# Performance work log

Hardware: AMD Instinct MI355X
Metric: run time of the kernel (lower is better)

## Reference

```python
import jax, jax.numpy as jnp
import numpy as np

HIDDEN = 512
HEADS = 8
HEAD_DIM = HIDDEN // HEADS
MAX_DIST = 10
B, N = 16, 512
EPS = 1e-5


def _layer_norm(x, g, b):
    mu = jnp.mean(x, axis=-1, keepdims=True)
    var = jnp.mean(jnp.square(x - mu), axis=-1, keepdims=True)
    return (x - mu) * jax.lax.rsqrt(var + EPS) * g + b


def setup_inputs() -> dict:
    key = jax.random.key(0)
    ks = jax.random.split(key, 16)
    s = 0.02
    inp = {
        "x": jax.random.normal(ks[0], (B, N, HIDDEN), jnp.float32),
        "distances": jax.random.randint(ks[1], (B, N, N), 0, MAX_DIST, jnp.int32),
        "edge_features": jax.random.normal(ks[2], (B, N, N), jnp.float32),
        "attn_mask": jax.random.randint(ks[3], (B, N), 0, 2).astype(bool),
        "Wq": jax.random.normal(ks[4], (HIDDEN, HIDDEN), jnp.float32) * s,
        "bq": jnp.zeros((HIDDEN,), jnp.float32),
        "Wk": jax.random.normal(ks[5], (HIDDEN, HIDDEN), jnp.float32) * s,
        "bk": jnp.zeros((HIDDEN,), jnp.float32),
        "Wv": jax.random.normal(ks[6], (HIDDEN, HIDDEN), jnp.float32) * s,
        "bv": jnp.zeros((HIDDEN,), jnp.float32),
        "Wo": jax.random.normal(ks[7], (HIDDEN, HIDDEN), jnp.float32) * s,
        "bo": jnp.zeros((HIDDEN,), jnp.float32),
        "spatial_emb": jax.random.normal(ks[8], (MAX_DIST, HEADS), jnp.float32) * s,
        "edge_w": jax.random.normal(ks[9], (HEADS,), jnp.float32) * s,
        "edge_b": jnp.zeros((HEADS,), jnp.float32),
        "ln1_g": jnp.ones((HIDDEN,), jnp.float32),
        "ln1_b": jnp.zeros((HIDDEN,), jnp.float32),
        "ln2_g": jnp.ones((HIDDEN,), jnp.float32),
        "ln2_b": jnp.zeros((HIDDEN,), jnp.float32),
        "W1": jax.random.normal(ks[10], (HIDDEN, 4 * HIDDEN), jnp.float32) * s,
        "b1": jnp.zeros((4 * HIDDEN,), jnp.float32),
        "W2": jax.random.normal(ks[11], (4 * HIDDEN, HIDDEN), jnp.float32) * s,
        "b2": jnp.zeros((HIDDEN,), jnp.float32),
    }
    return inp


def reference(x, distances, edge_features, attn_mask, Wq, bq, Wk, bk, Wv, bv,
              Wo, bo, spatial_emb, edge_w, edge_b, ln1_g, ln1_b, ln2_g, ln2_b,
              W1, b1, W2, b2):
    b, n, _ = x.shape
    q = (x @ Wq + bq).reshape(b, n, HEADS, HEAD_DIM)
    k = (x @ Wk + bk).reshape(b, n, HEADS, HEAD_DIM)
    v = (x @ Wv + bv).reshape(b, n, HEADS, HEAD_DIM)
    # [b, h, i, j] attention scores
    scores = jnp.einsum('bihd,bjhd->bhij', q, k) / np.sqrt(HEAD_DIM).astype(np.float32)
    spatial_bias = spatial_emb[distances]                       # [b, i, j, h]
    edge_bias = edge_features[..., None] * edge_w + edge_b      # [b, i, j, h]
    scores = scores + jnp.transpose(spatial_bias + edge_bias, (0, 3, 1, 2))
    scores = jnp.where(attn_mask[:, None, None, :], -jnp.inf, scores)
    attn = jax.nn.softmax(scores, axis=-1)
    out = jnp.einsum('bhij,bjhd->bihd', attn, v).reshape(b, n, HIDDEN)
    out = out @ Wo + bo
    h = _layer_norm(x + out, ln1_g, ln1_b)
    ffn = jax.nn.relu(h @ W1 + b1) @ W2 + b2
    return _layer_norm(h + ffn, ln2_g, ln2_b)
```

## Files before the change

### kernel.cpp

```cpp
#include <hip/hip_runtime.h>
#include <stdint.h>
#include <stddef.h>

#define SEQ   512
#define HID   512
#define NHEAD 8
#define HD    64
#define NBATCH 16
#define NTOK  8192
#define MAXD  10
#define LOG2E 1.4426950408889634f

typedef __attribute__((ext_vector_type(8))) short short8;
typedef __attribute__((ext_vector_type(4))) float f32x4;

typedef __attribute__((address_space(3))) void        as3_void;
typedef const __attribute__((address_space(1))) void  as1_cvoid;

#define MFMA16(a,b,c) __builtin_amdgcn_mfma_f32_16x16x32_bf16((a),(b),(c),0,0,0)

__device__ __forceinline__ float bf2f(uint16_t u){ return __uint_as_float(((uint32_t)u)<<16); }
__device__ __forceinline__ uint16_t f2bf(float f){
  uint32_t i = __float_as_uint(f);
  return (uint16_t)((i + 0x7fffu + ((i>>16)&1u)) >> 16);
}

enum { EPI_BF16=0, EPI_F32=3, EPI_RELU=4 };

__global__ __launch_bounds__(256) void f2bf_kernel(
    const float* __restrict__ in, uint16_t* __restrict__ out, int n4)
{
  int i = blockIdx.x*256 + threadIdx.x;
  if (i < n4){
    float4 v = *(const float4*)(in + (size_t)i*4);
    *(ushort4*)(out + (size_t)i*4) =
        make_ushort4(f2bf(v.x), f2bf(v.y), f2bf(v.z), f2bf(v.w));
  }
}

__global__ __launch_bounds__(256) void transpose_all(
    const float* __restrict__ Wq, const float* __restrict__ Wk,
    const float* __restrict__ Wv, const float* __restrict__ Wo,
    const float* __restrict__ W1, const float* __restrict__ W2,
    uint16_t* __restrict__ tq, uint16_t* __restrict__ tk,
    uint16_t* __restrict__ tv, uint16_t* __restrict__ to_,
    uint16_t* __restrict__ t1, uint16_t* __restrict__ t2)
{
  __shared__ uint16_t tile[32][33];
  int id = blockIdx.x;
  const float* in; uint16_t* out; int R, C, tx, ty;
  if (id < 1024) {
    int m = id >> 8, loc = id & 255;
    in  = (m==0)?Wq:(m==1)?Wk:(m==2)?Wv:Wo;
    out = (m==0)?tq:(m==1)?tk:(m==2)?tv:to_;
    R = 512; C = 512; ty = loc>>4; tx = loc&15;
  } else if (id < 2048) {
    int loc = id-1024; in=W1; out=t1; R=512; C=2048; ty=loc>>6; tx=loc&63;
  } else {
    int loc = id-2048; in=W2; out=t2; R=2048; C=512; ty=loc>>4; tx=loc&15;
  }
  int bx = tx*32, by = ty*32;
  int lx = threadIdx.x & 31, ly = threadIdx.x >> 5;
  #pragma unroll
  for (int i=ly; i<32; i+=8) tile[i][lx] = f2bf(in[(size_t)(by+i)*C + bx+lx]);
  __syncthreads();
  #pragma unroll
  for (int i=ly; i<32; i+=8) out[(size_t)(bx+i)*R + by+lx] = tile[lx][i];
}

__global__ __launch_bounds__(512) void pack_bias(
    const int*   __restrict__ dist,
    const float* __restrict__ edge,
    const int*   __restrict__ mask,
    uint32_t*    __restrict__ outp)
{
  __shared__ int   dl[16][260];
  __shared__ float el[16][260];
  __shared__ int   ml[512];
  const int b  = blockIdx.y;
  const int it = blockIdx.x;
  const int t  = threadIdx.x;
  ml[t] = mask[b*SEQ + t];

  #pragma unroll
  for (int jh=0; jh<2; ++jh){
    if (jh) __syncthreads();
    {
      const int r  = t >> 5;
      const int c0 = (t & 31) * 8;
      const size_t g = ((size_t)b*SEQ + it*16 + r)*SEQ + jh*256 + c0;
      *(int4*)&dl[r][c0]     = *(const int4*)&dist[g];
      *(int4*)&dl[r][c0+4]   = *(const int4*)&dist[g+4];
      *(float4*)&el[r][c0]   = *(const float4*)&edge[g];
      *(float4*)&el[r][c0+4] = *(const float4*)&edge[g+4];
    }
    __syncthreads();
    {
      const int i   = t & 15;
      const int j0p = (t >> 4) * 8;
      const int jt  = jh*4 + (j0p >> 6);
      const int jn  = (j0p >> 4) & 3;
      const int lg  = (j0p & 15) >> 2;
      uint32_t w[8];
      #pragma unroll
      for (int e=0; e<8; ++e){
        const int jl = j0p + e;
        const int jg = jh*256 + jl;
        const uint32_t d  = (uint32_t)dl[i][jl] & 0xFFu;
        const uint32_t mk = (ml[jg] ? 1u : 0u) << 8;
        w[e] = ((uint32_t)f2bf(el[i][jl]) << 16) | mk | d;
      }
      uint32_t* ob = outp + ((((size_t)b*32 + it)*8 + jt)*64)*16;
      const int lane0 = lg*16 + i, lane1 = (lg+1)*16 + i;
      *(uint4*)&ob[lane0*16 + jn*4] = make_uint4(w[0],w[1],w[2],w[3]);
      *(uint4*)&ob[lane1*16 + jn*4] = make_uint4(w[4],w[5],w[6],w[7]);
    }
  }
}

template<int BM, int BN>
__device__ __forceinline__ void gemm_tile_mainloop(
    const uint16_t* __restrict__ A, const uint16_t* __restrict__ Bt,
    int K, int m0, int n0, uint16_t* lA, uint16_t* lB,
    f32x4 acc[4][(BM==128)?4:((BN==128)?2:1)])
{
  constexpr int NJ  = (BM==128)?4:((BN==128)?2:1);
  constexpr int ARD = BM/32;
  constexpr int BRD = BN/32;
  constexpr bool DB = (BM==64) && (BN==64);
  const int t = threadIdx.x;
  const int w = t>>6, l = t&63;
  const int lg = l>>4, lc = l&15;
  const int wr = (BM==128)?(w>>1):0;
  const int wc = (BM==128)?(w&1):w;
  const int swz = lc & 7;
  const int kSteps = K>>6;

  auto stage = [&](int kt, int buf){
    const int k0 = kt<<6;
    #pragma unroll
    for (int rd=0; rd<ARD; ++rd){
      const int e   = rd*2048 + t*8;
      const int row = e>>6;
      const int col = (((e>>3)&7) ^ (row&7))*8;
      const uint16_t* ga = A + (size_t)(m0+row)*K + (k0+col);
      char* la = (char*)(lA + buf*(BM*64)) + rd*4096 + w*1024;
      __builtin_amdgcn_global_load_lds((as1_cvoid*)ga, (as3_void*)la, 16, 0, 0);
    }
    #pragma unroll
    for (int rd=0; rd<BRD; ++rd){
      const int e   = rd*2048 + t*8;
      const int row = e>>6;
      const int col = (((e>>3)&7) ^ (row&7))*8;
      const uint16_t* gb = Bt + (size_t)(n0+row)*K + (k0+col);
      char* lb = (char*)(lB + buf*(BN*64)) + rd*4096 + w*1024;
      __builtin_amdgcn_global_load_lds((as1_cvoid*)gb, (as3_void*)lb, 16, 0, 0);
    }
  };

  auto compute = [&](const uint16_t* rA, const uint16_t* rB){
    #pragma unroll
    for (int kk=0; kk<2; ++kk){
      const int cc = (kk*4 + lg) ^ swz;
      short8 af[4], bfr[NJ];
      #pragma unroll
      for (int i=0;i<4;i++)
        af[i]  = *(const short8*)&rA[(wr*64 + i*16 + lc)*64 + cc*8];
      #pragma unroll
      for (int j=0;j<NJ;j++)
        bfr[j] = *(const short8*)&rB[(wc*16*NJ + j*16 + lc)*64 + cc*8];
      #pragma unroll
      for (int i=0;i<4;i++)
        #pragma unroll
        for (int j=0;j<NJ;j++)
          acc[i][j] = MFMA16(af[i], bfr[j], acc[i][j]);
    }
  };

  if constexpr (DB){
    stage(0, 0);
    __syncthreads();
    int cur = 0;
    for (int kt=0; kt<kSteps; ++kt){
      if (kt+1 < kSteps) stage(kt+1, cur^1);
      compute(lA + cur*(BM*64), lB + cur*(BN*64));
      __syncthreads();
      cur ^= 1;
    }
  } else {
    for (int kt=0; kt<kSteps; ++kt){
      stage(kt, 0);
      __syncthreads();
      compute(lA, lB);
      __syncthreads();
    }
  }
}

template<int EPI, int BM, int BN>
__global__ __launch_bounds__(256,2) void gemm_bt(
    const uint16_t* __restrict__ A, const uint16_t* __restrict__ Bt,
    const float* __restrict__ bias, void* __restrict__ outp,
    int M, int N, int K)
{
  constexpr int NJ = (BM==128)?4:((BN==128)?2:1);
  constexpr int NB = ((BM==64)&&(BN==64)) ? 2 : 1;
  __shared__ uint16_t lA[NB*BM*64];
  __shared__ uint16_t lB[NB*BN*64];
  f32x4 acc[4][NJ];
  #pragma unroll
  for (int i=0;i<4;i++)
    #pragma unroll
    for (int j=0;j<NJ;j++){ f32x4 z = {0.f,0.f,0.f,0.f}; acc[i][j]=z; }
  const int m0 = blockIdx.x*BM, n0 = blockIdx.y*BN;
  gemm_tile_mainloop<BM,BN>(A, Bt, K, m0, n0, lA, lB, acc);

  const int t=threadIdx.x, w=t>>6, l=t&63, lg=l>>4, lc=l&15;
  const int wr=(BM==128)?(w>>1):0, wc=(BM==128)?(w&1):w;
  #pragma unroll
  for (int j=0;j<NJ;j++){
    const int col = n0 + wc*16*NJ + j*16 + lc;
    const float bs = bias[col];
    #pragma unroll
    for (int i=0;i<4;i++){
      const int rowb = m0 + wr*64 + i*16 + lg*4;
      #pragma unroll
      for (int r=0;r<4;r++){
        float v = acc[i][j][r] + bs;
        if constexpr (EPI==EPI_RELU)   v = fmaxf(v, 0.f);
        if constexpr (EPI==EPI_F32)
          ((float*)outp)[(size_t)(rowb+r)*N + col] = v;
        else
          ((uint16_t*)outp)[(size_t)(rowb+r)*N + col] = f2bf(v);
      }
    }
  }
}

__global__ __launch_bounds__(256,2) void qkv_gemm(
    const uint16_t* __restrict__ x,
    const uint16_t* __restrict__ wtq, const uint16_t* __restrict__ wtk,
    const uint16_t* __restrict__ wtv,
    const float* __restrict__ bq, const float* __restrict__ bk,
    const float* __restrict__ bv,
    uint16_t* __restrict__ qo, uint16_t* __restrict__ kp,
    uint16_t* __restrict__ vp)
{
  __shared__ uint16_t lA[2*64*64];
  __shared__ uint16_t lB[2*64*64];
  const int z = blockIdx.z;
  const uint16_t* Bt = (z==0)?wtq:(z==1)?wtk:wtv;
  const float*  bias = (z==0)?bq :(z==1)?bk :bv;
  f32x4 acc[4][1];
  #pragma unroll
  for (int i=0;i<4;i++){ f32x4 zz = {0.f,0.f,0.f,0.f}; acc[i][0]=zz; }
  const int m0 = blockIdx.x*64, n0 = blockIdx.y*64;
  gemm_tile_mainloop<64,64>(x, Bt, HID, m0, n0, lA, lB, acc);

  const int t=threadIdx.x, w=t>>6, l=t&63, lg=l>>4, lc=l&15;
  const int col = n0 + w*16 + lc;
  if (z==0){
    const float scale = 0.125f * LOG2E;
    const float bs = bias[col];
    #pragma unroll
    for (int i=0;i<4;i++){
      const int rowb = m0 + i*16 + lg*4;
      #pragma unroll
      for (int r=0;r<4;r++)
        qo[(size_t)(rowb+r)*HID + col] = f2bf((acc[i][0][r] + bs)*scale);
    }
  } else if (z==1){
    const float bs = bias[col];
    const int h_ = col>>6, cm = col&63, kk = cm>>5, lgk = (cm>>3)&3, e = col&7;
    #pragma unroll
    for (int i=0;i<4;i++){
      const int rowb = m0 + i*16 + lg*4;
      #pragma unroll
      for (int r=0;r<4;r++){
        const int tok = rowb + r;
        const int b_ = tok>>9, tl = tok&511;
        const int jt = tl>>6, jn = (tl>>4)&3, lck = tl&15;
        kp[((((size_t)(b_*8+h_)*8 + jt)*4 + jn)*2 + kk)*512
           + (lgk*16 + lck)*8 + e] = f2bf(acc[i][0][r] + bs);
      }
    }
  } else {
    const float bs = bias[col];
    const int h_ = col>>6, dn = (col>>4)&3, lcv = col&15;
    #pragma unroll
    for (int i=0;i<4;i++){
      const int rowb = m0 + i*16 + lg*4;
      const int b_ = rowb>>9, tl = rowb&511;
      const int jt = tl>>6, kk = (tl>>5)&1, lgv = (tl>>3)&3, e0 = tl&7;
      *(ushort4*)&vp[((((size_t)(b_*8+h_)*8 + jt)*2 + kk)*4 + dn)*512
                     + (lgv*16 + lcv)*8 + e0] =
          make_ushort4(f2bf(acc[i][0][0]+bs), f2bf(acc[i][0][1]+bs),
                       f2bf(acc[i][0][2]+bs), f2bf(acc[i][0][3]+bs));
    }
  }
}

__global__ __launch_bounds__(512,4) void attn_kernel(
    const uint16_t* __restrict__ q,
    const uint16_t* __restrict__ kp,
    const uint16_t* __restrict__ vp,
    const uint32_t* __restrict__ biasp,
    const float*    __restrict__ semb,
    const float*    __restrict__ ew,
    const float*    __restrict__ eb,
    uint16_t* __restrict__ out)
{
  __shared__ float sp_rep[NHEAD][32][11];
  __shared__ uint16_t plds[NHEAD][2][16*72];
  const int b  = blockIdx.y;
  const int it = blockIdx.x;
  const int i0 = it*16;
  const int t  = threadIdx.x;
  const int h  = t>>6, l = t&63, lg = l>>4, lc = l&15;
  for (int i = t; i < NHEAD*32*MAXD; i += 512){
    const int hh = i / (32*MAXD), rem = i % (32*MAXD);
    const int a = rem / MAXD, d = rem % MAXD;
    sp_rep[hh][a][d] = (semb[d*NHEAD + hh] + eb[hh]) * LOG2E;
  }
  __syncthreads();
  const float ewf = ew[h] * LOG2E;
  const float* spl = &sp_rep[h][l&31][0];
  char* pbase = (char*)&plds[h][0][0] + lc*144;

  short8 qf[2];
  #pragma unroll
  for (int kk=0;kk<2;kk++)
    qf[kk] = *(const short8*)&q[(size_t)(b*SEQ + i0 + lc)*HID + h*HD + kk*32 + lg*8];

  const uint4* bp = (const uint4*)(biasp + (((size_t)b*32 + it)*8)*64*16);
  const uint16_t* kpb = kp + (size_t)(b*8+h)*8*4*2*512 + l*8;
  const uint16_t* vpb = vp + (size_t)(b*8+h)*8*2*4*512 + l*8;

  float mrun[2] = {-1e30f, -1e30f};
  float lrun[2] = {0.f, 0.f};
  f32x4 oacc[2][4];
  #pragma unroll
  for (int s=0;s<2;s++)
    #pragma unroll
    for (int dn=0;dn<4;dn++){ f32x4 z={0.f,0.f,0.f,0.f}; oacc[s][dn]=z; }

  #pragma unroll
  for (int p=0; p<4; ++p){
    #pragma unroll
    for (int s=0; s<2; ++s){
      const int jt = s*4 + p;
      uint32_t uw[16];
      {
        const uint4* bq_ = bp + (jt*64 + l)*4;
        *(uint4*)&uw[0]  = bq_[0];
        *(uint4*)&uw[4]  = bq_[1];
        *(uint4*)&uw[8]  = bq_[2];
        *(uint4*)&uw[12] = bq_[3];
      }
      f32x4 st[4];
      #pragma unroll
      for (int jn=0;jn<4;jn++){ f32x4 z={0.f,0.f,0.f,0.f}; st[jn]=z; }
      __builtin_amdgcn_s_setprio(1);
      #pragma unroll
      for (int jn=0;jn<4;jn++){
        #pragma unroll
        for (int kk=0;kk<2;kk++){
          short8 kf = *(const short8*)&kpb[(size_t)((jt*4 + jn)*2 + kk)*512];
          st[jn] = MFMA16(kf, qf[kk], st[jn]);
        }
      }
      __builtin_amdgcn_s_setprio(0);
      float tmax = -1e30f;
      #pragma unroll
      for (int jn=0;jn<4;jn++){
        #pragma unroll
        for (int r=0;r<4;r++){
          const uint32_t u = uw[jn*4+r];
          float sv = st[jn][r] + spl[u & 0xFFu]
                   + bf2f((uint16_t)(u >> 16))*ewf;
          if (u & 0x100u) sv = -1e30f;
          st[jn][r] = sv;
          tmax = fmaxf(tmax, sv);
        }
      }
      {
        float tm = fmaxf(tmax, __shfl_xor(tmax, 16, 64));
        tm = fmaxf(tm, __shfl_xor(tm, 32, 64));
        float mnew = fmaxf(mrun[s], tm);
        mnew = fmaxf(mnew, -1e20f);
        const float c = __builtin_amdgcn_exp2f(mrun[s] - mnew);
        mrun[s] = mnew;
        float lsum = 0.f;
        char* pb = pbase + s*(16*72*2);
        #pragma unroll
        for (int jn=0;jn<4;jn++){
          float p0 = __builtin_amdgcn_exp2f(st[jn][0]-mnew);
          float p1 = __builtin_amdgcn_exp2f(st[jn][1]-mnew);
          float p2 = __builtin_amdgcn_exp2f(st[jn][2]-mnew);
          float p3 = __builtin_amdgcn_exp2f(st[jn][3]-mnew);
          lsum += (p0+p1)+(p2+p3);
          *(ushort4*)(pb + (jn*16 + lg*4)*2) =
              make_ushort4(f2bf(p0), f2bf(p1), f2bf(p2), f2bf(p3));
        }
        lrun[s] = lrun[s]*c + lsum;
        #pragma unroll
        for (int r=0;r<4;r++){
          const float cr = __shfl(c, lg*4+r, 64);
          #pragma unroll
          for (int dn=0;dn<4;dn++) oacc[s][dn][r] *= cr;
        }
      }
    }
    #pragma unroll
    for (int s=0; s<2; ++s){
      const int jt = s*4 + p;
      char* pb = pbase + s*(16*72*2);
      __builtin_amdgcn_s_setprio(1);
      #pragma unroll
      for (int kk=0;kk<2;kk++){
        short8 pa = *(const short8*)(pb + (kk*32 + lg*8)*2);
        #pragma unroll
        for (int dn=0;dn<4;dn++){
          short8 vb = *(const short8*)&vpb[(size_t)((jt*2 + kk)*4 + dn)*512];
          oacc[s][dn] = MFMA16(pa, vb, oacc[s][dn]);
        }
      }
      __builtin_amdgcn_s_setprio(0);
    }
  }
  {
    const float mm = fmaxf(mrun[0], mrun[1]);
    const float c0 = __builtin_amdgcn_exp2f(mrun[0]-mm);
    const float c1 = __builtin_amdgcn_exp2f(mrun[1]-mm);
    float ls = lrun[0]*c0 + lrun[1]*c1;
    ls += __shfl_xor(ls, 16, 64);
    ls += __shfl_xor(ls, 32, 64);
    const float inv = 1.f/ls;
    #pragma unroll
    for (int r=0;r<4;r++){
      const float cr0 = __shfl(c0, lg*4+r, 64);
      const float cr1 = __shfl(c1, lg*4+r, 64);
      const float ir  = __shfl(inv, lg*4+r, 64);
      const size_t orow = ((size_t)b*SEQ + i0 + lg*4 + r)*HID;
      #pragma unroll
      for (int dn=0;dn<4;dn++)
        out[orow + h*HD + dn*16 + lc] =
            f2bf((oacc[0][dn][r]*cr0 + oacc[1][dn][r]*cr1)*ir);
    }
  }
}

__global__ __launch_bounds__(256) void ln_kernel(
    const uint16_t* __restrict__ a, const float* __restrict__ bsrc,
    const float* __restrict__ g, const float* __restrict__ bb,
    float* __restrict__ of, uint16_t* __restrict__ ob)
{
  const int row = blockIdx.x*4 + (threadIdx.x>>6);
  const int l = threadIdx.x & 63;
  const int c0 = l*8;
  const uint16_t* ar = a    + (size_t)row*HID + c0;
  const float*    br = bsrc + (size_t)row*HID + c0;
  short8 av = *(const short8*)ar;
  float4 b0 = *(const float4*)br;
  float4 b1 = *(const float4*)(br+4);
  float u[8];
  u[0]=bf2f((uint16_t)av[0])+b0.x; u[1]=bf2f((uint16_t)av[1])+b0.y;
  u[2]=bf2f((uint16_t)av[2])+b0.z; u[3]=bf2f((uint16_t)av[3])+b0.w;
  u[4]=bf2f((uint16_t)av[4])+b1.x; u[5]=bf2f((uint16_t)av[5])+b1.y;
  u[6]=bf2f((uint16_t)av[6])+b1.z; u[7]=bf2f((uint16_t)av[7])+b1.w;
  float s=0.f, ss=0.f;
  #pragma unroll
  for (int e=0;e<8;e++){ s += u[e]; ss += u[e]*u[e]; }
  #pragma unroll
  for (int off=32; off>=1; off>>=1){
    s  += __shfl_xor(s,  off, 64);
    ss += __shfl_xor(ss, off, 64);
  }
  const float mu  = s*(1.f/512.f);
  const float inv = rsqrtf(ss*(1.f/512.f) - mu*mu + 1e-5f);
  float4 g0 = *(const float4*)(g + c0),  g1 = *(const float4*)(g + c0 + 4);
  float4 q0 = *(const float4*)(bb + c0), q1 = *(const float4*)(bb + c0 + 4);
  float y[8];
  y[0]=(u[0]-mu)*inv*g0.x+q0.x; y[1]=(u[1]-mu)*inv*g0.y+q0.y;
  y[2]=(u[2]-mu)*inv*g0.z+q0.z; y[3]=(u[3]-mu)*inv*g0.w+q0.w;
  y[4]=(u[4]-mu)*inv*g1.x+q1.x; y[5]=(u[5]-mu)*inv*g1.y+q1.y;
  y[6]=(u[6]-mu)*inv*g1.z+q1.z; y[7]=(u[7]-mu)*inv*g1.w+q1.w;
  if (of){
    float* orow = of + (size_t)row*HID + c0;
    *(float4*)orow     = make_float4(y[0],y[1],y[2],y[3]);
    *(float4*)(orow+4) = make_float4(y[4],y[5],y[6],y[7]);
  }
  if (ob){
    uint16_t* brow = ob + (size_t)row*HID + c0;
    *(ushort4*)brow     = make_ushort4(f2bf(y[0]),f2bf(y[1]),f2bf(y[2]),f2bf(y[3]));
    *(ushort4*)(brow+4) = make_ushort4(f2bf(y[4]),f2bf(y[5]),f2bf(y[6]),f2bf(y[7]));
  }
}

extern "C" void kernel_launch(void* const* d_in, const int* in_sizes, int n_in,
                              void* d_out, int out_size, void* d_ws, size_t ws_size,
                              hipStream_t stream)
{
  (void)in_sizes; (void)n_in; (void)out_size; (void)ws_size;
  const float* x    = (const float*)d_in[0];
  const int*   dist = (const int*)  d_in[1];
  const float* edge = (const float*)d_in[2];
  const int*   mask = (const int*)  d_in[3];
  const float* Wq = (const float*)d_in[4];
  const float* bq = (const float*)d_in[5];
  const float* Wk = (const float*)d_in[6];
  const float* bk = (const float*)d_in[7];
  const float* Wv = (const float*)d_in[8];
  const float* bv = (const float*)d_in[9];
  const float* Wo = (const float*)d_in[10];
  const float* bo = (const float*)d_in[11];
  const float* semb = (const float*)d_in[12];
  const float* ew   = (const float*)d_in[13];
  const float* eb   = (const float*)d_in[14];
  const float* ln1g = (const float*)d_in[15];
  const float* ln1b = (const float*)d_in[16];
  const float* ln2g = (const float*)d_in[17];
  const float* ln2b = (const float*)d_in[18];
  const float* W1 = (const float*)d_in[19];
  const float* b1 = (const float*)d_in[20];
  const float* W2 = (const float*)d_in[21];
  const float* b2 = (const float*)d_in[22];

  char* ws = (char*)d_ws;
  uint16_t* xb16  = (uint16_t*)ws;
  uint16_t* qbuf  = xb16  + (size_t)NTOK*HID;
  uint16_t* kpbuf = qbuf  + (size_t)NTOK*HID;
  uint16_t* vpbuf = kpbuf + (size_t)NTOK*HID;
  uint16_t* aobuf = vpbuf + (size_t)NTOK*HID;
  uint16_t* f1buf = qbuf;
  uint32_t* biasp = (uint32_t*)(ws + (size_t)5*NTOK*HID*2);
  uint16_t* tb16  = (uint16_t*)biasp;
  uint16_t* t2b16 = tb16;
  float*    hbuf  = (float*)((char*)biasp + (size_t)NTOK*HID*4);
  uint16_t* hb16  = (uint16_t*)(hbuf + (size_t)NTOK*HID);
  uint16_t* wt    = hb16 + (size_t)NTOK*HID;
  uint16_t* wtq = wt;
  uint16_t* wtk = wtq + 512*512;
  uint16_t* wtv = wtk + 512*512;
  uint16_t* wto = wtv + 512*512;
  uint16_t* wt1 = wto + 512*512;
  uint16_t* wt2 = wt1 + 512*2048;

  pack_bias<<<dim3(32,16), 512, 0, stream>>>(dist, edge, mask, biasp);

  transpose_all<<<3072, 256, 0, stream>>>(Wq,Wk,Wv,Wo,W1,W2, wtq,wtk,wtv,wto,wt1,wt2);

  f2bf_kernel<<<4096, 256, 0, stream>>>(x, xb16, NTOK*HID/4);

  qkv_gemm<<<dim3(128,8,3), 256, 0, stream>>>(xb16, wtq,wtk,wtv, bq,bk,bv,
                                              qbuf, kpbuf, vpbuf);

  attn_kernel<<<dim3(32,16), 512, 0, stream>>>(qbuf, kpbuf, vpbuf, biasp,
                                               semb, ew, eb, aobuf);

  gemm_bt<EPI_BF16,64,64><<<dim3(128,8), 256, 0, stream>>>(aobuf, wto, bo, tb16, NTOK, HID, HID);

  ln_kernel<<<2048, 256, 0, stream>>>(tb16, x, ln1g, ln1b, hbuf, hb16);

  gemm_bt<EPI_RELU,64,64><<<dim3(128,32), 256, 0, stream>>>(hb16, wt1, b1, f1buf, NTOK, 2048, HID);

  gemm_bt<EPI_BF16,64,64><<<dim3(128,8), 256, 0, stream>>>(f1buf, wt2, b2, t2b16, NTOK, HID, 2048);

  ln_kernel<<<2048, 256, 0, stream>>>(t2b16, hbuf, ln2g, ln2b, (float*)d_out, nullptr);
}
```

Measured before the change: 171.6 us.

## Use 128x128 tiles for QKV and FFN1 GEMMs, swizzle attention P LDS

The QKV projection and the first FFN GEMM now use 128x128 block tiles with a 4x4 accumulator grid per wave, which cuts redundant global loads and raises MFMA work per LDS fetch. The QKV epilogue is rewritten to loop over the extra column fragments. Separately, the attention kernel's P staging buffer drops the row padding and uses an XOR swizzle to avoid LDS bank conflicts while using less shared memory. The larger tiles raise register use and leave fewer blocks in flight, which may reduce occupancy.

```diff
diff --git a/kernel.cpp b/kernel.cpp
--- a/kernel.cpp
+++ b/kernel.cpp
@@ -246,56 +246,69 @@
     uint16_t* __restrict__ qo, uint16_t* __restrict__ kp,
     uint16_t* __restrict__ vp)
 {
-  __shared__ uint16_t lA[2*64*64];
-  __shared__ uint16_t lB[2*64*64];
+  __shared__ uint16_t lA[128*64];
+  __shared__ uint16_t lB[128*64];
   const int z = blockIdx.z;
   const uint16_t* Bt = (z==0)?wtq:(z==1)?wtk:wtv;
   const float*  bias = (z==0)?bq :(z==1)?bk :bv;
-  f32x4 acc[4][1];
-  #pragma unroll
-  for (int i=0;i<4;i++){ f32x4 zz = {0.f,0.f,0.f,0.f}; acc[i][0]=zz; }
-  const int m0 = blockIdx.x*64, n0 = blockIdx.y*64;
-  gemm_tile_mainloop<64,64>(x, Bt, HID, m0, n0, lA, lB, acc);
-
-  const int t=threadIdx.x, w=t>>6, l=t&63, lg=l>>4, lc=l&15;
-  const int col = n0 + w*16 + lc;
+  f32x4 acc[4][4];
+  #pragma unroll
+  for (int i=0;i<4;i++)
+    #pragma unroll
+    for (int j=0;j<4;j++){ f32x4 zz = {0.f,0.f,0.f,0.f}; acc[i][j]=zz; }
+  const int m0 = blockIdx.x*128, n0 = blockIdx.y*128;
+  gemm_tile_mainloop<128,128>(x, Bt, HID, m0, n0, lA, lB, acc);
+
+  const int t=threadIdx.x, w=t>>6, l=t&63, lg=l>>4, lc=l&15, wr=w>>1, wc=w&1;
   if (z==0){
     const float scale = 0.125f * LOG2E;
-    const float bs = bias[col];
-    #pragma unroll
-    for (int i=0;i<4;i++){
-      const int rowb = m0 + i*16 + lg*4;
-      #pragma unroll
-      for (int r=0;r<4;r++)
-        qo[(size_t)(rowb+r)*HID + col] = f2bf((acc[i][0][r] + bs)*scale);
+    #pragma unroll
+    for (int j=0;j<4;j++){
+      const int col = n0 + wc*64 + j*16 + lc;
+      const float bs = bias[col];
+      #pragma unroll
+      for (int i=0;i<4;i++){
+        const int rowb = m0 + wr*64 + i*16 + lg*4;
+        #pragma unroll
+        for (int r=0;r<4;r++)
+          qo[(size_t)(rowb+r)*HID + col] = f2bf((acc[i][j][r] + bs)*scale);
+      }
     }
   } else if (z==1){
-    const float bs = bias[col];
-    const int h_ = col>>6, cm = col&63, kk = cm>>5, lgk = (cm>>3)&3, e = col&7;
-    #pragma unroll
-    for (int i=0;i<4;i++){
-      const int rowb = m0 + i*16 + lg*4;
-      #pragma unroll
-      for (int r=0;r<4;r++){
-        const int tok = rowb + r;
-        const int b_ = tok>>9, tl = tok&511;
-        const int jt = tl>>6, jn = (tl>>4)&3, lck = tl&15;
-        kp[((((size_t)(b_*8+h_)*8 + jt)*4 + jn)*2 + kk)*512
-           + (lgk*16 + lck)*8 + e] = f2bf(acc[i][0][r] + bs);
+    #pragma unroll
+    for (int j=0;j<4;j++){
+      const int col = n0 + wc*64 + j*16 + lc;
+      const float bs = bias[col];
+      const int h_ = col>>6, cm = col&63, kk = cm>>5, lgk = (cm>>3)&3, e = col&7;
+      #pragma unroll
+      for (int i=0;i<4;i++){
+        const int rowb = m0 + wr*64 + i*16 + lg*4;
+        #pragma unroll
+        for (int r=0;r<4;r++){
+          const int tok = rowb + r;
+          const int b_ = tok>>9, tl = tok&511;
+          const int jt = tl>>6, jn = (tl>>4)&3, lck = tl&15;
+          kp[((((size_t)(b_*8+h_)*8 + jt)*4 + jn)*2 + kk)*512
+             + (lgk*16 + lck)*8 + e] = f2bf(acc[i][j][r] + bs);
+        }
       }
     }
   } else {
-    const float bs = bias[col];
-    const int h_ = col>>6, dn = (col>>4)&3, lcv = col&15;
-    #pragma unroll
-    for (int i=0;i<4;i++){
-      const int rowb = m0 + i*16 + lg*4;
-      const int b_ = rowb>>9, tl = rowb&511;
-      const int jt = tl>>6, kk = (tl>>5)&1, lgv = (tl>>3)&3, e0 = tl&7;
-      *(ushort4*)&vp[((((size_t)(b_*8+h_)*8 + jt)*2 + kk)*4 + dn)*512
-                     + (lgv*16 + lcv)*8 + e0] =
-          make_ushort4(f2bf(acc[i][0][0]+bs), f2bf(acc[i][0][1]+bs),
-                       f2bf(acc[i][0][2]+bs), f2bf(acc[i][0][3]+bs));
+    #pragma unroll
+    for (int j=0;j<4;j++){
+      const int col = n0 + wc*64 + j*16 + lc;
+      const float bs = bias[col];
+      const int h_ = col>>6, dn = (col>>4)&3, lcv = col&15;
+      #pragma unroll
+      for (int i=0;i<4;i++){
+        const int rowb = m0 + wr*64 + i*16 + lg*4;
+        const int b_ = rowb>>9, tl = rowb&511;
+        const int jt = tl>>6, kk = (tl>>5)&1, lgv = (tl>>3)&3, e0 = tl&7;
+        *(ushort4*)&vp[((((size_t)(b_*8+h_)*8 + jt)*2 + kk)*4 + dn)*512
+                       + (lgv*16 + lcv)*8 + e0] =
+            make_ushort4(f2bf(acc[i][j][0]+bs), f2bf(acc[i][j][1]+bs),
+                         f2bf(acc[i][j][2]+bs), f2bf(acc[i][j][3]+bs));
+      }
     }
   }
 }
@@ -311,7 +324,7 @@
     uint16_t* __restrict__ out)
 {
   __shared__ float sp_rep[NHEAD][32][11];
-  __shared__ uint16_t plds[NHEAD][2][16*72];
+  __shared__ uint16_t plds[NHEAD][2][16*64];
   const int b  = blockIdx.y;
   const int it = blockIdx.x;
   const int i0 = it*16;
@@ -325,7 +338,8 @@
   __syncthreads();
   const float ewf = ew[h] * LOG2E;
   const float* spl = &sp_rep[h][l&31][0];
-  char* pbase = (char*)&plds[h][0][0] + lc*144;
+  char* pbase = (char*)&plds[h][0][0];
+  const int swz = (lc&7)<<4;
 
   short8 qf[2];
   #pragma unroll
@@ -391,7 +405,7 @@
         const float c = __builtin_amdgcn_exp2f(mrun[s] - mnew);
         mrun[s] = mnew;
         float lsum = 0.f;
-        char* pb = pbase + s*(16*72*2);
+        char* pb = pbase + s*(16*64*2) + lc*128;
         #pragma unroll
         for (int jn=0;jn<4;jn++){
           float p0 = __builtin_amdgcn_exp2f(st[jn][0]-mnew);
@@ -399,7 +413,7 @@
           float p2 = __builtin_amdgcn_exp2f(st[jn][2]-mnew);
           float p3 = __builtin_amdgcn_exp2f(st[jn][3]-mnew);
           lsum += (p0+p1)+(p2+p3);
-          *(ushort4*)(pb + (jn*16 + lg*4)*2) =
+          *(ushort4*)(pb + (((jn*16 + lg*4)*2) ^ swz)) =
               make_ushort4(f2bf(p0), f2bf(p1), f2bf(p2), f2bf(p3));
         }
         lrun[s] = lrun[s]*c + lsum;
@@ -414,11 +428,11 @@
     #pragma unroll
     for (int s=0; s<2; ++s){
       const int jt = s*4 + p;
-      char* pb = pbase + s*(16*72*2);
+      char* pb = pbase + s*(16*64*2) + lc*128;
       __builtin_amdgcn_s_setprio(1);
       #pragma unroll
       for (int kk=0;kk<2;kk++){
-        short8 pa = *(const short8*)(pb + (kk*32 + lg*8)*2);
+        short8 pa = *(const short8*)(pb + (((kk*32 + lg*8)*2) ^ swz));
         #pragma unroll
         for (int dn=0;dn<4;dn++){
           short8 vb = *(const short8*)&vpb[(size_t)((jt*2 + kk)*4 + dn)*512];
@@ -552,8 +566,8 @@
 
   f2bf_kernel<<<4096, 256, 0, stream>>>(x, xb16, NTOK*HID/4);
 
-  qkv_gemm<<<dim3(128,8,3), 256, 0, stream>>>(xb16, wtq,wtk,wtv, bq,bk,bv,
-                                              qbuf, kpbuf, vpbuf);
+  qkv_gemm<<<dim3(64,4,3), 256, 0, stream>>>(xb16, wtq,wtk,wtv, bq,bk,bv,
+                                             qbuf, kpbuf, vpbuf);
 
   attn_kernel<<<dim3(32,16), 512, 0, stream>>>(qbuf, kpbuf, vpbuf, biasp,
                                                semb, ew, eb, aobuf);
@@ -562,7 +576,7 @@
 
   ln_kernel<<<2048, 256, 0, stream>>>(tb16, x, ln1g, ln1b, hbuf, hb16);
 
-  gemm_bt<EPI_RELU,64,64><<<dim3(128,32), 256, 0, stream>>>(hb16, wt1, b1, f1buf, NTOK, 2048, HID);
+  gemm_bt<EPI_RELU,128,128><<<dim3(64,16), 256, 0, stream>>>(hb16, wt1, b1, f1buf, NTOK, 2048, HID);
 
   gemm_bt<EPI_BF16,64,64><<<dim3(128,8), 256, 0, stream>>>(f1buf, wt2, b2, t2b16, NTOK, HID, 2048);
 
```

New measurement: 160.4 us. 6.5% less time.
